# Performance work log

Measured on AMD Instinct MI355X. Metric: run time of the kernel, lower is better.

Reference implementation:

```python
import jax, jax.numpy as jnp
import numpy as np

N_NODES = 50000


def gcn_conv(x, src, dst, W, b):
    # PyG GCNConv: h = D^-1/2 (A+I) D^-1/2 (x W) + b, aggregation at dst.
    n = x.shape[0]
    deg = jax.ops.segment_sum(jnp.ones_like(dst, dtype=x.dtype), dst, num_segments=n)
    dinv = jnp.where(deg > 0, jax.lax.rsqrt(deg), 0.0)
    norm = dinv[src] * dinv[dst]                      # [E]
    h = x @ W                                         # [N, out]
    msg = h[src] * norm[:, None]                      # [E, out] gather
    out = jax.ops.segment_sum(msg, dst, num_segments=n)  # scatter-add
    return out + b


def setup_inputs() -> dict:
    key = jax.random.key(0)
    k1, k2, k3, k4 = jax.random.split(key, 4)
    in_dim, hid, out_dim = 128, 256, 128
    x = jax.random.normal(k1, (N_NODES, in_dim), dtype=jnp.float32)
    edge_index = jax.random.randint(k2, (2, 800000), 0, N_NODES, dtype=jnp.int64)
    s1 = 1.0 / np.sqrt(in_dim)
    s2 = 1.0 / np.sqrt(hid)
    W1 = jax.random.uniform(k3, (in_dim, hid), jnp.float32, -s1, s1)
    b1 = jnp.zeros((hid,), jnp.float32)
    W2 = jax.random.uniform(k4, (hid, out_dim), jnp.float32, -s2, s2)
    b2 = jnp.zeros((out_dim,), jnp.float32)
    return {"x": x, "edge_index": edge_index, "W1": W1, "b1": b1, "W2": W2, "b2": b2}


def reference(x, edge_index, W1, b1, W2, b2):
    n = x.shape[0]
    loops = jnp.arange(n, dtype=edge_index.dtype)
    src = jnp.concatenate([edge_index[0], loops])  # add self-loops
    dst = jnp.concatenate([edge_index[1], loops])
    h = jax.nn.relu(gcn_conv(x, src, dst, W1, b1))
    # dropout in eval mode -> identity
    return gcn_conv(h, src, dst, W2, b2)
```

## Files before the change

kernel.cpp:

```cpp
#include <hip/hip_runtime.h>
#include <hip/hip_bf16.h>


typedef __bf16 bf16x8v __attribute__((ext_vector_type(8)));
typedef short  s16x8   __attribute__((ext_vector_type(8)));
typedef float  f32x4   __attribute__((ext_vector_type(4)));

#define IN_DIM 128
#define HID    256
#define OUTD   128
#define BKT_SHIFT 7
#define BKT_NODES 128
#define MAXB 512
#define CAP  2560
#define EBLK 512

__device__ __forceinline__ float2 bf2f(__hip_bfloat162 v) {
    return make_float2(__bfloat162float(v.x), __bfloat162float(v.y));
}
__device__ __forceinline__ __hip_bfloat162 f2bf(float a, float b) {
    __hip_bfloat162 r; r.x = __float2bfloat16(a); r.y = __float2bfloat16(b); return r;
}
__device__ __forceinline__ void acc_row(float* acc, s16x8 r) {
    __hip_bfloat162* p = (__hip_bfloat162*)&r;
#pragma unroll
    for (int j = 0; j < 4; ++j) {
        float2 f = bf2f(p[j]);
        acc[2 * j]     += f.x;
        acc[2 * j + 1] += f.y;
    }
}

__device__ __forceinline__ int detect_f32(const void* W2raw) {
    const unsigned short* u = (const unsigned short*)W2raw;
    int f32 = 0;
#pragma unroll
    for (int i = 0; i < 64; ++i) {
        unsigned e = (u[i] >> 7) & 0xFF;
        if (e >= 0x7F) f32 = 1;
    }
    return f32;
}
__device__ __forceinline__ int detect_i64(const void* eiraw) {
    const unsigned* ip = (const unsigned*)eiraw;
    unsigned orodd = 0;
#pragma unroll
    for (int i = 0; i < 64; ++i) orodd |= ip[2 * i + 1];
    return (orodd == 0) ? 1 : 0;
}

__device__ __forceinline__ short ldw(const void* raw, int idx, int f32) {
    if (f32) {
        __hip_bfloat16 h = __float2bfloat16(((const float*)raw)[idx]);
        return *(short*)&h;
    }
    return ((const short*)raw)[idx];
}

template <int K, int NN>
__device__ __forceinline__ void swz_one(const void* Wraw, int f32,
                                        short* __restrict__ Bsw, int tid) {
    constexpr int KC = K / 32;
    constexpr int NT = NN / 16;
    if (tid >= NT * KC * 64) return;
    int lane = tid & 63;
    int kc   = (tid >> 6) % KC;
    int nt   = tid / (64 * KC);
    int n  = nt * 16 + (lane & 15);
    int kb = kc * 32 + (lane >> 4) * 8;
    s16x8 v;
#pragma unroll
    for (int j = 0; j < 8; ++j) v[j] = ldw(Wraw, (kb + j) * NN + n, f32);
    ((s16x8*)Bsw)[tid] = v;
}


__global__ __launch_bounds__(256) void k_pe(
        const void* __restrict__ ei_, int E, int N, int NB,
        int* __restrict__ bcnt, unsigned* __restrict__ ppack,
        const void* W1raw, const void* b1raw, const void* W2raw, const void* b2raw,
        short* __restrict__ Bsw1, short* __restrict__ Bsw2,
        __hip_bfloat16* __restrict__ b1c, __hip_bfloat16* __restrict__ b2c,
        int* __restrict__ flags) {
    int blk = blockIdx.x, t = threadIdx.x;
    if (blk >= EBLK) {
        int f32 = detect_f32(W2raw);
        int pb = blk - EBLK;
        if (pb < 16) {
            swz_one<IN_DIM, HID>(W1raw, f32, Bsw1, pb * 256 + t);
        } else if (pb < 32) {
            swz_one<HID, OUTD>(W2raw, f32, Bsw2, (pb - 16) * 256 + t);
        } else {
            short s1 = ldw(b1raw, t, f32);
            b1c[t] = *(__hip_bfloat16*)&s1;
            if (t < OUTD) {
                short s2 = ldw(b2raw, t, f32);
                b2c[t] = *(__hip_bfloat16*)&s2;
            }
            if (t == 0) {
                flags[0] = f32;
                flags[1] = detect_i64(ei_);
            }
        }
        return;
    }
    __shared__ int lhist[4][MAXB];
    __shared__ int lbase[4][MAXB];
    int wv = t >> 6;
    int i64 = detect_i64(ei_);
    const long long* p64 = (const long long*)ei_;
    const int*       p32 = (const int*)ei_;
    int per = (E + EBLK - 1) / EBLK;
    int e0 = blk * per, e1 = min(e0 + per, E);
    for (int i = t; i < NB; i += 256) {
        lhist[0][i] = 0; lhist[1][i] = 0; lhist[2][i] = 0; lhist[3][i] = 0;
    }
    __syncthreads();
    for (int e = e0 + t; e < e1; e += 256) {
        int d = i64 ? (int)p64[E + e] : p32[E + e];
        if ((unsigned)d >= (unsigned)N) d = 0;
        atomicAdd(&lhist[wv][((unsigned)d) >> BKT_SHIFT], 1);
    }
    __syncthreads();
    for (int i = t; i < NB; i += 256) {
        int c0 = lhist[0][i], c1 = lhist[1][i], c2 = lhist[2][i], c3 = lhist[3][i];
        int tot = c0 + c1 + c2 + c3;
        int g = tot ? atomicAdd(&bcnt[i], tot) : 0;
        lbase[0][i] = g;
        lbase[1][i] = g + c0;
        lbase[2][i] = g + c0 + c1;
        lbase[3][i] = g + c0 + c1 + c2;
        lhist[0][i] = 0; lhist[1][i] = 0; lhist[2][i] = 0; lhist[3][i] = 0;
    }
    __syncthreads();
    for (int e = e0 + t; e < e1; e += 256) {
        int d = i64 ? (int)p64[E + e] : p32[E + e];
        int s = i64 ? (int)p64[e]     : p32[e];
        if ((unsigned)d >= (unsigned)N) d = 0;
        if ((unsigned)s >= (unsigned)N) s = 0;
        int b = ((unsigned)d) >> BKT_SHIFT;
        int pos = lbase[wv][b] + atomicAdd(&lhist[wv][b], 1);
        if (pos < CAP) {
            unsigned pk = ((unsigned)(d & (BKT_NODES - 1)) << 25) | (unsigned)s;
            __builtin_nontemporal_store(pk, &ppack[(size_t)b * CAP + pos]);
        }
    }
}


__global__ __launch_bounds__(512) void k_bsort(const int* __restrict__ bcnt,
                                               const unsigned* __restrict__ ppack,
                                               int NB,
                                               int* __restrict__ csr, int* __restrict__ offsets,
                                               float* __restrict__ dinv, int N,
                                               const void* __restrict__ xraw,
                                               const int* __restrict__ flags,
                                               __hip_bfloat16* __restrict__ xs) {
    __shared__ int sb[MAXB];
    __shared__ int h[BKT_NODES], base[BKT_NODES], s[BKT_NODES];
    __shared__ float sdv[BKT_NODES];
    int b = blockIdx.x;
    int t = threadIdx.x;
    int c = (t < NB) ? min(bcnt[t], CAP) : 0;
    sb[t] = c;
    __syncthreads();
    for (int off = 1; off < MAXB; off <<= 1) {
        int u = (t >= off) ? sb[t - off] : 0;
        __syncthreads();
        sb[t] += u;
        __syncthreads();
    }
    int cnt   = min(bcnt[b], CAP);
    int ebase = sb[b] - cnt;
    if (b == NB - 1 && t == 0) offsets[N] = sb[b];
    const unsigned* pp = ppack + (size_t)b * CAP;
    if (t < BKT_NODES) h[t] = 0;
    __syncthreads();
    for (int e = t; e < cnt; e += 512) atomicAdd(&h[pp[e] >> 25], 1);
    __syncthreads();
    int v = (t < BKT_NODES) ? h[t] : 0;
    if (t < BKT_NODES) s[t] = v;
    __syncthreads();
    for (int off = 1; off < BKT_NODES; off <<= 1) {
        int u = (t < BKT_NODES && t >= off) ? s[t - off] : 0;
        __syncthreads();
        if (t < BKT_NODES) s[t] += u;
        __syncthreads();
    }
    if (t < BKT_NODES) {
        int excl = s[t] - v;
        base[t] = excl;
        int node = b * BKT_NODES + t;
        float dv = 0.f;
        if (node < N) {
            dv = rsqrtf((float)(v + 1));
            offsets[node] = ebase + excl;
            dinv[node] = dv;
        } else {
            dinv[node] = 0.f;
        }
        sdv[t] = dv;
        h[t] = 0;
    }
    __syncthreads();
    for (int e = t; e < cnt; e += 512) {
        unsigned pk = pp[e];
        int ld = pk >> 25;
        int pos = ebase + base[ld] + atomicAdd(&h[ld], 1);
        csr[pos] = (int)(pk & 0x1FFFFFFu);
    }
    int f32 = flags[0];
    if (!f32) {
        const s16x8* xg = (const s16x8*)xraw;
        s16x8* xo = (s16x8*)xs;
        for (int u = t; u < BKT_NODES * 16; u += 512) {
            int row = u >> 4;
            int node = b * BKT_NODES + row;
            float dv = sdv[row];
            s16x8 val = {0, 0, 0, 0, 0, 0, 0, 0};
            if (node < N) {
                s16x8 xin = xg[(size_t)node * 16 + (u & 15)];
                __hip_bfloat162* xp = (__hip_bfloat162*)&xin;
                __hip_bfloat162* vp = (__hip_bfloat162*)&val;
#pragma unroll
                for (int j = 0; j < 4; ++j) {
                    float2 f = bf2f(xp[j]);
                    vp[j] = f2bf(dv * f.x, dv * f.y);
                }
            }
            xo[(size_t)node * 16 + (u & 15)] = val;
        }
    } else {
        const float4* xg = (const float4*)xraw;
        __hip_bfloat162* xo = (__hip_bfloat162*)xs;
        for (int u = t; u < BKT_NODES * 32; u += 512) {
            int row = u >> 5;
            int node = b * BKT_NODES + row;
            float dv = sdv[row];
            __hip_bfloat162 v0 = f2bf(0.f, 0.f), v1 = v0;
            if (node < N) {
                float4 xin = xg[(size_t)node * 32 + (u & 31)];
                v0 = f2bf(dv * xin.x, dv * xin.y);
                v1 = f2bf(dv * xin.z, dv * xin.w);
            }
            xo[(size_t)node * 64 + (u & 31) * 2]     = v0;
            xo[(size_t)node * 64 + (u & 31) * 2 + 1] = v1;
        }
    }
}


__global__ __launch_bounds__(256) void k_agg1(
        const s16x8* __restrict__ xs8, const int* __restrict__ offsets,
        const int* __restrict__ csr, const float* __restrict__ dinv,
        s16x8* __restrict__ a8, int N, int Npad) {
    int gw   = blockIdx.x * 4 + (threadIdx.x >> 6);
    int lane = threadIdx.x & 63;
    int quad = lane >> 4, l16 = lane & 15;
    int v = gw * 4 + quad;
    if (v >= Npad) return;
    const char* xb = (const char*)xs8;
    unsigned go = ((unsigned)v << 8) | ((unsigned)l16 << 4);
    if (v >= N) {
        s16x8 z = {0, 0, 0, 0, 0, 0, 0, 0};
        *(s16x8*)((char*)a8 + go) = z;
        return;
    }
    float acc[8];
#pragma unroll
    for (int j = 0; j < 8; ++j) acc[j] = 0.f;
    int o0 = offsets[v], o1 = offsets[v + 1];
    acc_row(acc, *(const s16x8*)(xb + go));
    int e = o0;
    for (; e + 3 < o1; e += 4) {
        int s0 = __builtin_nontemporal_load(&csr[e]);
        int s1 = __builtin_nontemporal_load(&csr[e + 1]);
        int s2 = __builtin_nontemporal_load(&csr[e + 2]);
        int s3 = __builtin_nontemporal_load(&csr[e + 3]);
        s16x8 r0 = *(const s16x8*)(xb + (((unsigned)s0 << 8) | ((unsigned)l16 << 4)));
        s16x8 r1 = *(const s16x8*)(xb + (((unsigned)s1 << 8) | ((unsigned)l16 << 4)));
        s16x8 r2 = *(const s16x8*)(xb + (((unsigned)s2 << 8) | ((unsigned)l16 << 4)));
        s16x8 r3 = *(const s16x8*)(xb + (((unsigned)s3 << 8) | ((unsigned)l16 << 4)));
        acc_row(acc, r0); acc_row(acc, r1); acc_row(acc, r2); acc_row(acc, r3);
    }
    for (; e < o1; ++e) {
        int s0 = __builtin_nontemporal_load(&csr[e]);
        acc_row(acc, *(const s16x8*)(xb + (((unsigned)s0 << 8) | ((unsigned)l16 << 4))));
    }
    float dv = dinv[v];
    s16x8 outv;
    __hip_bfloat162* op = (__hip_bfloat162*)&outv;
#pragma unroll
    for (int j = 0; j < 4; ++j) op[j] = f2bf(dv * acc[2 * j], dv * acc[2 * j + 1]);
    *(s16x8*)((char*)a8 + go) = outv;
}


__global__ __launch_bounds__(256) void k_gemm12(
        const __hip_bfloat16* __restrict__ A, const __hip_bfloat16* __restrict__ Bsw1,
        const __hip_bfloat16* __restrict__ b1c, const __hip_bfloat16* __restrict__ Bsw2,
        const float* __restrict__ dinv, __hip_bfloat16* __restrict__ h2s) {
    __shared__ __align__(16) __hip_bfloat16 at[64 * IN_DIM];
    __shared__ __align__(16) __hip_bfloat16 hl[64 * HID];
    int wave = threadIdx.x >> 6, lane = threadIdx.x & 63;
    int quad = lane >> 4, l16 = lane & 15;
    int gm0 = blockIdx.x * 64;

    {
        int row = wave * 16 + l16;
        const s16x8* Ar = (const s16x8*)(A + (size_t)(gm0 + row) * IN_DIM);
#pragma unroll
        for (int k = 0; k < 4; ++k) {
            int g = quad + 4 * k;
            s16x8 vv = Ar[g];
            *(s16x8*)((char*)at + (((unsigned)row << 8) | ((unsigned)(g ^ (row & 15)) << 4))) = vv;
        }
    }
    __syncthreads();

    const bf16x8v* B1 = reinterpret_cast<const bf16x8v*>(Bsw1);
    for (int nt = wave * 4; nt < wave * 4 + 4; ++nt) {
        bf16x8v bfr[4];
#pragma unroll
        for (int kc = 0; kc < 4; ++kc) bfr[kc] = B1[(nt * 4 + kc) * 64 + lane];
        int col = nt * 16 + l16;
        float bv = __bfloat162float(b1c[col]);
        int gcol = col >> 3, csub = col & 7;
#pragma unroll
        for (int rs = 0; rs < 4; ++rs) {
            int arow = rs * 16 + l16;
            f32x4 acc = {0.f, 0.f, 0.f, 0.f};
#pragma unroll
            for (int kc = 0; kc < 4; ++kc) {
                bf16x8v af = *reinterpret_cast<const bf16x8v*>(
                    (char*)at + (((unsigned)arow << 8) | ((unsigned)((kc * 4 + quad) ^ (arow & 15)) << 4)));
                acc = __builtin_amdgcn_mfma_f32_16x16x32_bf16(af, bfr[kc], acc, 0, 0, 0);
            }
#pragma unroll
            for (int r = 0; r < 4; ++r) {
                float v0 = acc[r] + bv; v0 = v0 > 0.f ? v0 : 0.f;
                int r0 = rs * 16 + quad * 4 + r;
                ((__hip_bfloat16*)((char*)hl + (size_t)r0 * (HID * 2) + ((gcol ^ (r0 & 31)) << 4)))[csub] = __float2bfloat16(v0);
            }
        }
    }
    __syncthreads();

    const bf16x8v* B2 = reinterpret_cast<const bf16x8v*>(Bsw2);
    for (int nt = wave * 2; nt < wave * 2 + 2; ++nt) {
        bf16x8v b2r[8];
#pragma unroll
        for (int kc = 0; kc < 8; ++kc) b2r[kc] = B2[(nt * 8 + kc) * 64 + lane];
        int col = nt * 16 + l16;
#pragma unroll
        for (int rs = 0; rs < 4; ++rs) {
            int arow = rs * 16 + l16;
            f32x4 acc = {0.f, 0.f, 0.f, 0.f};
#pragma unroll
            for (int kc = 0; kc < 8; ++kc) {
                bf16x8v af = *reinterpret_cast<const bf16x8v*>(
                    (char*)hl + (size_t)arow * (HID * 2) + ((size_t)((kc * 4 + quad) ^ (arow & 31)) << 4));
                acc = __builtin_amdgcn_mfma_f32_16x16x32_bf16(af, b2r[kc], acc, 0, 0, 0);
            }
            int rb = gm0 + rs * 16 + quad * 4;
#pragma unroll
            for (int r = 0; r < 4; ++r) {
                float sc = dinv[rb + r];
                h2s[(size_t)(rb + r) * OUTD + col] = __float2bfloat16(acc[r] * sc);
            }
        }
    }
}


__global__ __launch_bounds__(256) void k_agg2(
        const s16x8* __restrict__ h8, const int* __restrict__ offsets,
        const int* __restrict__ csr, const float* __restrict__ dinv,
        const __hip_bfloat16* __restrict__ b2c, const int* __restrict__ flags,
        void* __restrict__ outraw, int N) {
    int gw   = blockIdx.x * 4 + (threadIdx.x >> 6);
    int lane = threadIdx.x & 63;
    int quad = lane >> 4, l16 = lane & 15;
    int f32 = flags[0];
    const char* hb = (const char*)h8;
    float bb[8];
    {
        s16x8 bv = ((const s16x8*)b2c)[l16];
        __hip_bfloat162* bp = (__hip_bfloat162*)&bv;
#pragma unroll
        for (int j = 0; j < 4; ++j) {
            float2 f = bf2f(bp[j]);
            bb[2 * j] = f.x; bb[2 * j + 1] = f.y;
        }
    }
    int v = gw * 4 + quad;
    if (v >= N) return;
    float acc[8];
#pragma unroll
    for (int j = 0; j < 8; ++j) acc[j] = 0.f;
    int o0 = offsets[v], o1 = offsets[v + 1];
    acc_row(acc, *(const s16x8*)(hb + (((unsigned)v << 8) | ((unsigned)l16 << 4))));
    int e = o0;
    for (; e + 3 < o1; e += 4) {
        int s0 = __builtin_nontemporal_load(&csr[e]);
        int s1 = __builtin_nontemporal_load(&csr[e + 1]);
        int s2 = __builtin_nontemporal_load(&csr[e + 2]);
        int s3 = __builtin_nontemporal_load(&csr[e + 3]);
        s16x8 r0 = *(const s16x8*)(hb + (((unsigned)s0 << 8) | ((unsigned)l16 << 4)));
        s16x8 r1 = *(const s16x8*)(hb + (((unsigned)s1 << 8) | ((unsigned)l16 << 4)));
        s16x8 r2 = *(const s16x8*)(hb + (((unsigned)s2 << 8) | ((unsigned)l16 << 4)));
        s16x8 r3 = *(const s16x8*)(hb + (((unsigned)s3 << 8) | ((unsigned)l16 << 4)));
        acc_row(acc, r0); acc_row(acc, r1); acc_row(acc, r2); acc_row(acc, r3);
    }
    for (; e < o1; ++e) {
        int s0 = __builtin_nontemporal_load(&csr[e]);
        acc_row(acc, *(const s16x8*)(hb + (((unsigned)s0 << 8) | ((unsigned)l16 << 4))));
    }
    float dv = dinv[v];
    if (f32) {
        f32x4* of = (f32x4*)outraw;
        f32x4 o0v = {dv * acc[0] + bb[0], dv * acc[1] + bb[1],
                     dv * acc[2] + bb[2], dv * acc[3] + bb[3]};
        f32x4 o1v = {dv * acc[4] + bb[4], dv * acc[5] + bb[5],
                     dv * acc[6] + bb[6], dv * acc[7] + bb[7]};
        __builtin_nontemporal_store(o0v, &of[(size_t)v * 32 + l16 * 2]);
        __builtin_nontemporal_store(o1v, &of[(size_t)v * 32 + l16 * 2 + 1]);
    } else {
        s16x8 outv;
        __hip_bfloat162* op = (__hip_bfloat162*)&outv;
#pragma unroll
        for (int j = 0; j < 4; ++j)
            op[j] = f2bf(dv * acc[2 * j] + bb[2 * j], dv * acc[2 * j + 1] + bb[2 * j + 1]);
        __builtin_nontemporal_store(outv, &((s16x8*)outraw)[(size_t)v * 16 + l16]);
    }
}


extern "C" void kernel_launch(void* const* d_in, const int* in_sizes, int n_in,
                              void* d_out, int out_size, void* d_ws, size_t ws_size,
                              hipStream_t stream) {
    const void* x  = d_in[0];
    const void* ei = d_in[1];
    const void* W1 = d_in[2];
    const void* b1 = d_in[3];
    const void* W2 = d_in[4];
    const void* b2 = d_in[5];

    const int N = in_sizes[0] / IN_DIM;
    const int E = in_sizes[1] / 2;
    const int Npad = ((N + 127) / 128) * 128;
    const int NB = Npad / BKT_NODES;

    char* w = (char*)d_ws;
    auto alloc = [&](size_t bytes) -> void* {
        void* p = (void*)w;
        w += (bytes + 255) / 256 * 256;
        return p;
    };
    int*   flags   = (int*)alloc(256);
    int*   bcnt    = (int*)alloc((size_t)MAXB * 4);
    int*   offsets = (int*)alloc((size_t)(N + 1) * 4);
    float* dinv    = (float*)alloc((size_t)Npad * 4);
    unsigned* ppack = (unsigned*)alloc((size_t)NB * CAP * 4);
    int*   csr     = (int*)alloc((size_t)E * 4);
    short* Bsw1 = (short*)alloc((size_t)IN_DIM * HID * 2);
    short* Bsw2 = (short*)alloc((size_t)HID * OUTD * 2);
    __hip_bfloat16* b1c = (__hip_bfloat16*)alloc((size_t)HID * 2);
    __hip_bfloat16* b2c = (__hip_bfloat16*)alloc((size_t)OUTD * 2);
    __hip_bfloat16* xs  = (__hip_bfloat16*)alloc((size_t)Npad * IN_DIM * 2);
    __hip_bfloat16* a1  = (__hip_bfloat16*)alloc((size_t)Npad * IN_DIM * 2);
    __hip_bfloat16* h2s = xs;

    hipMemsetAsync(bcnt, 0, (size_t)MAXB * 4, stream);

    k_pe<<<EBLK + 33, 256, 0, stream>>>(ei, E, N, NB, bcnt, ppack,
                                        W1, b1, W2, b2, Bsw1, Bsw2, b1c, b2c, flags);

    k_bsort<<<NB, 512, 0, stream>>>(bcnt, ppack, NB, csr, offsets, dinv, N,
                                    x, flags, xs);

    k_agg1<<<Npad / 16, 256, 0, stream>>>((const s16x8*)xs, offsets, csr, dinv,
                                          (s16x8*)a1, N, Npad);

    k_gemm12<<<Npad / 64, 256, 0, stream>>>(a1, (const __hip_bfloat16*)Bsw1, b1c,
                                            (const __hip_bfloat16*)Bsw2, dinv, h2s);

    const int agg2Blocks = (N + 15) / 16;
    k_agg2<<<agg2Blocks, 256, 0, stream>>>((const s16x8*)h2s, offsets, csr, dinv,
                                           b2c, flags, d_out, N);
}
```

Baseline: 214.5 us.

## Merge edge partitioning and bucket sort into one cooperative kernel with grid sync

The edge bucketing kernel and the per-bucket sort kernel become a single cooperative launch that separates the two phases with a grid-wide barrier. The grid shrinks to NB+17 blocks of 512 threads, and the weight swizzle work moves after the barrier into the extra blocks. The intent is to remove one kernel launch and its inter-kernel gap. The risks are that the edge histogram phase now runs on fewer blocks (about 408 instead of 512), the grid barrier has its own cost, and cooperative launch limits residency.

```diff
diff --git a/kernel.cpp b/kernel.cpp
--- a/kernel.cpp
+++ b/kernel.cpp
@@ -1,5 +1,8 @@
 #include <hip/hip_runtime.h>
 #include <hip/hip_bf16.h>
+#include <hip/hip_cooperative_groups.h>
+
+namespace cg = cooperative_groups;
 
 
 typedef __bf16 bf16x8v __attribute__((ext_vector_type(8)));
@@ -13,7 +16,6 @@
 #define BKT_NODES 128
 #define MAXB 512
 #define CAP  2560
-#define EBLK 512
 
 __device__ __forceinline__ float2 bf2f(__hip_bfloat162 v) {
     return make_float2(__bfloat162float(v.x), __bfloat162float(v.y));
@@ -75,24 +77,77 @@
 }
 
 
-__global__ __launch_bounds__(256) void k_pe(
+__global__ __launch_bounds__(512, 4) void k_prep(
         const void* __restrict__ ei_, int E, int N, int NB,
         int* __restrict__ bcnt, unsigned* __restrict__ ppack,
         const void* W1raw, const void* b1raw, const void* W2raw, const void* b2raw,
         short* __restrict__ Bsw1, short* __restrict__ Bsw2,
         __hip_bfloat16* __restrict__ b1c, __hip_bfloat16* __restrict__ b2c,
-        int* __restrict__ flags) {
+        int* __restrict__ flags,
+        int* __restrict__ csr, int* __restrict__ offsets, float* __restrict__ dinv,
+        const void* __restrict__ xraw, __hip_bfloat16* __restrict__ xs) {
+    __shared__ __align__(16) int smem[4096];
     int blk = blockIdx.x, t = threadIdx.x;
-    if (blk >= EBLK) {
+    int nblk = gridDim.x;
+
+    {
+        int (*lhist)[MAXB] = (int(*)[MAXB])smem;
+        int (*lbase)[MAXB] = (int(*)[MAXB])(smem + 2048);
+        int wv = (t >> 6) & 3;
+        int i64 = detect_i64(ei_);
+        const long long* p64 = (const long long*)ei_;
+        const int*       p32 = (const int*)ei_;
+        int per = (E + nblk - 1) / nblk;
+        int e0 = blk * per, e1 = min(e0 + per, E);
+        for (int i = t; i < NB; i += 512) {
+            lhist[0][i] = 0; lhist[1][i] = 0; lhist[2][i] = 0; lhist[3][i] = 0;
+        }
+        __syncthreads();
+        for (int e = e0 + t; e < e1; e += 512) {
+            int d = i64 ? (int)p64[E + e] : p32[E + e];
+            if ((unsigned)d >= (unsigned)N) d = 0;
+            atomicAdd(&lhist[wv][((unsigned)d) >> BKT_SHIFT], 1);
+        }
+        __syncthreads();
+        for (int i = t; i < NB; i += 512) {
+            int c0 = lhist[0][i], c1 = lhist[1][i], c2 = lhist[2][i], c3 = lhist[3][i];
+            int tot = c0 + c1 + c2 + c3;
+            int g = tot ? atomicAdd(&bcnt[i], tot) : 0;
+            lbase[0][i] = g;
+            lbase[1][i] = g + c0;
+            lbase[2][i] = g + c0 + c1;
+            lbase[3][i] = g + c0 + c1 + c2;
+            lhist[0][i] = 0; lhist[1][i] = 0; lhist[2][i] = 0; lhist[3][i] = 0;
+        }
+        __syncthreads();
+        for (int e = e0 + t; e < e1; e += 512) {
+            int d = i64 ? (int)p64[E + e] : p32[E + e];
+            int s = i64 ? (int)p64[e]     : p32[e];
+            if ((unsigned)d >= (unsigned)N) d = 0;
+            if ((unsigned)s >= (unsigned)N) s = 0;
+            int b = ((unsigned)d) >> BKT_SHIFT;
+            int pos = lbase[wv][b] + atomicAdd(&lhist[wv][b], 1);
+            if (pos < CAP) {
+                unsigned pk = ((unsigned)(d & (BKT_NODES - 1)) << 25) | (unsigned)s;
+                __builtin_nontemporal_store(pk, &ppack[(size_t)b * CAP + pos]);
+            }
+        }
+    }
+    __threadfence();
+    cg::this_grid().sync();
+
+    if (blk >= NB) {
+        int pb = blk - NB;
         int f32 = detect_f32(W2raw);
-        int pb = blk - EBLK;
-        if (pb < 16) {
-            swz_one<IN_DIM, HID>(W1raw, f32, Bsw1, pb * 256 + t);
-        } else if (pb < 32) {
-            swz_one<HID, OUTD>(W2raw, f32, Bsw2, (pb - 16) * 256 + t);
+        if (pb < 8) {
+            swz_one<IN_DIM, HID>(W1raw, f32, Bsw1, pb * 512 + t);
+        } else if (pb < 16) {
+            swz_one<HID, OUTD>(W2raw, f32, Bsw2, (pb - 8) * 512 + t);
         } else {
-            short s1 = ldw(b1raw, t, f32);
-            b1c[t] = *(__hip_bfloat16*)&s1;
+            if (t < HID) {
+                short s1 = ldw(b1raw, t, f32);
+                b1c[t] = *(__hip_bfloat16*)&s1;
+            }
             if (t < OUTD) {
                 short s2 = ldw(b2raw, t, f32);
                 b2c[t] = *(__hip_bfloat16*)&s2;
@@ -104,63 +159,13 @@
         }
         return;
     }
-    __shared__ int lhist[4][MAXB];
-    __shared__ int lbase[4][MAXB];
-    int wv = t >> 6;
-    int i64 = detect_i64(ei_);
-    const long long* p64 = (const long long*)ei_;
-    const int*       p32 = (const int*)ei_;
-    int per = (E + EBLK - 1) / EBLK;
-    int e0 = blk * per, e1 = min(e0 + per, E);
-    for (int i = t; i < NB; i += 256) {
-        lhist[0][i] = 0; lhist[1][i] = 0; lhist[2][i] = 0; lhist[3][i] = 0;
-    }
-    __syncthreads();
-    for (int e = e0 + t; e < e1; e += 256) {
-        int d = i64 ? (int)p64[E + e] : p32[E + e];
-        if ((unsigned)d >= (unsigned)N) d = 0;
-        atomicAdd(&lhist[wv][((unsigned)d) >> BKT_SHIFT], 1);
-    }
-    __syncthreads();
-    for (int i = t; i < NB; i += 256) {
-        int c0 = lhist[0][i], c1 = lhist[1][i], c2 = lhist[2][i], c3 = lhist[3][i];
-        int tot = c0 + c1 + c2 + c3;
-        int g = tot ? atomicAdd(&bcnt[i], tot) : 0;
-        lbase[0][i] = g;
-        lbase[1][i] = g + c0;
-        lbase[2][i] = g + c0 + c1;
-        lbase[3][i] = g + c0 + c1 + c2;
-        lhist[0][i] = 0; lhist[1][i] = 0; lhist[2][i] = 0; lhist[3][i] = 0;
-    }
-    __syncthreads();
-    for (int e = e0 + t; e < e1; e += 256) {
-        int d = i64 ? (int)p64[E + e] : p32[E + e];
-        int s = i64 ? (int)p64[e]     : p32[e];
-        if ((unsigned)d >= (unsigned)N) d = 0;
-        if ((unsigned)s >= (unsigned)N) s = 0;
-        int b = ((unsigned)d) >> BKT_SHIFT;
-        int pos = lbase[wv][b] + atomicAdd(&lhist[wv][b], 1);
-        if (pos < CAP) {
-            unsigned pk = ((unsigned)(d & (BKT_NODES - 1)) << 25) | (unsigned)s;
-            __builtin_nontemporal_store(pk, &ppack[(size_t)b * CAP + pos]);
-        }
-    }
-}
-
-
-__global__ __launch_bounds__(512) void k_bsort(const int* __restrict__ bcnt,
-                                               const unsigned* __restrict__ ppack,
-                                               int NB,
-                                               int* __restrict__ csr, int* __restrict__ offsets,
-                                               float* __restrict__ dinv, int N,
-                                               const void* __restrict__ xraw,
-                                               const int* __restrict__ flags,
-                                               __hip_bfloat16* __restrict__ xs) {
-    __shared__ int sb[MAXB];
-    __shared__ int h[BKT_NODES], base[BKT_NODES], s[BKT_NODES];
-    __shared__ float sdv[BKT_NODES];
-    int b = blockIdx.x;
-    int t = threadIdx.x;
+
+    int* sb   = smem;
+    int* h    = smem + 512;
+    int* base = smem + 640;
+    int* s    = smem + 768;
+    float* sdv = (float*)(smem + 896);
+    int b = blk;
     int c = (t < NB) ? min(bcnt[t], CAP) : 0;
     sb[t] = c;
     __syncthreads();
@@ -209,7 +214,7 @@
         int pos = ebase + base[ld] + atomicAdd(&h[ld], 1);
         csr[pos] = (int)(pk & 0x1FFFFFFu);
     }
-    int f32 = flags[0];
+    int f32 = detect_f32(W2raw);
     if (!f32) {
         const s16x8* xg = (const s16x8*)xraw;
         s16x8* xo = (s16x8*)xs;
@@ -446,10 +451,10 @@
     const void* W2 = d_in[4];
     const void* b2 = d_in[5];
 
-    const int N = in_sizes[0] / IN_DIM;
-    const int E = in_sizes[1] / 2;
+    int N = in_sizes[0] / IN_DIM;
+    int E = in_sizes[1] / 2;
     const int Npad = ((N + 127) / 128) * 128;
-    const int NB = Npad / BKT_NODES;
+    int NB = Npad / BKT_NODES;
 
     char* w = (char*)d_ws;
     auto alloc = [&](size_t bytes) -> void* {
@@ -471,13 +476,18 @@
     __hip_bfloat16* a1  = (__hip_bfloat16*)alloc((size_t)Npad * IN_DIM * 2);
     __hip_bfloat16* h2s = xs;
 
-    hipMemsetAsync(bcnt, 0, (size_t)MAXB * 4, stream);
-
-    k_pe<<<EBLK + 33, 256, 0, stream>>>(ei, E, N, NB, bcnt, ppack,
-                                        W1, b1, W2, b2, Bsw1, Bsw2, b1c, b2c, flags);
-
-    k_bsort<<<NB, 512, 0, stream>>>(bcnt, ppack, NB, csr, offsets, dinv, N,
-                                    x, flags, xs);
+    (void)hipMemsetAsync(bcnt, 0, (size_t)MAXB * 4, stream);
+
+    const int GRID = NB + 17;
+    void* args[] = {(void*)&ei, (void*)&E, (void*)&N, (void*)&NB,
+                    (void*)&bcnt, (void*)&ppack,
+                    (void*)&W1, (void*)&b1, (void*)&W2, (void*)&b2,
+                    (void*)&Bsw1, (void*)&Bsw2, (void*)&b1c, (void*)&b2c,
+                    (void*)&flags,
+                    (void*)&csr, (void*)&offsets, (void*)&dinv,
+                    (void*)&x, (void*)&xs};
+    (void)hipLaunchCooperativeKernel((const void*)k_prep, dim3(GRID), dim3(512),
+                                     args, 0, stream);
 
     k_agg1<<<Npad / 16, 256, 0, stream>>>((const s16x8*)xs, offsets, csr, dinv,
                                           (s16x8*)a1, N, Npad);
```

Result: slower. 374.2 us (+74.5%).
